# Performance work log

Measured on AMD Instinct MI355X. Metric: run time of the kernel, lower is better.

The kernel has to match this reference:

```python
import jax, jax.numpy as jnp
import numpy as np
from jax import lax

K = 3          # kernel_size
G = 2          # num_groups
DN = ('NHWC', 'HWIO', 'NHWC')


def _conv_same(x, w, b, groups=1):
    y = lax.conv_general_dilated(x, w, (1, 1), 'SAME',
                                 dimension_numbers=DN,
                                 feature_group_count=groups)
    return y + b


def _kernel_grid():
    off = (K - 1) / 2.0
    lin = jnp.linspace(-off, off, K, dtype=jnp.float32)
    dx, dy = jnp.meshgrid(lin, lin)              # 'xy' indexing, like tf default
    return jnp.stack([dx, dy], axis=-1).reshape(K * K, 2)  # [K2, 2] (dx, dy)


def _bilinear_sample(inp, loc):
    # inp: [B,H,W,C], loc: [B,H,W,K2,2] with (x,y) already clipped to valid range
    B, H, W, C = inp.shape
    x, y = loc[..., 0], loc[..., 1]
    x0 = jnp.floor(x); y0 = jnp.floor(y)
    x1 = jnp.clip(x0 + 1.0, 0.0, W - 1.0); x0 = jnp.clip(x0, 0.0, W - 1.0)
    y1 = jnp.clip(y0 + 1.0, 0.0, H - 1.0); y0 = jnp.clip(y0, 0.0, H - 1.0)
    # corner weights (computed from clipped coords, matching the TF code)
    wa = (x1 - x) * (y1 - y)
    wb = (x1 - x) * (y - y0)
    wc = (x - x0) * (y1 - y)
    wd = (x - x0) * (y - y0)
    x0i = x0.astype(jnp.int32); x1i = x1.astype(jnp.int32)
    y0i = y0.astype(jnp.int32); y1i = y1.astype(jnp.int32)
    flat = inp.reshape(B, H * W, C)

    def gather(yi, xi):
        idx = (yi * W + xi).reshape(B, -1, 1)               # [B, H*W*K2, 1]
        v = jnp.take_along_axis(flat, idx, axis=1)          # [B, H*W*K2, C]
        return v.reshape(B, H, W, K * K, C)

    out = (wa[..., None] * gather(y0i, x0i) + wb[..., None] * gather(y1i, x0i)
           + wc[..., None] * gather(y0i, x1i) + wd[..., None] * gather(y1i, x1i))
    return out  # [B,H,W,K2,C]


def _forward(x, off_w, off_b, dw_w, dw_b, pw_w, pw_b):
    B, H, W, C = x.shape
    Cg = C // G
    kg = _kernel_grid()                                     # [K2,2]
    gx, gy = jnp.meshgrid(jnp.arange(W, dtype=jnp.float32),
                          jnp.arange(H, dtype=jnp.float32))
    grid = jnp.stack([gx, gy], axis=-1)                     # [H,W,2] (x,y)
    outs = []
    for g in range(G):
        xi = x[..., g * Cg:(g + 1) * Cg]                    # [B,H,W,Cg]
        offsets = _conv_same(xi, off_w[g], off_b[g])        # [B,H,W,2*K2]
        offsets = offsets.reshape(B, H, W, K * K, 2)
        loc = grid[None, :, :, None, :] + kg[None, None, None] + offsets
        loc = jnp.stack([jnp.clip(loc[..., 0], 0.0, W - 1.0),
                         jnp.clip(loc[..., 1], 0.0, H - 1.0)], axis=-1)
        sampled = _bilinear_sample(xi, loc)                 # [B,H,W,K2,Cg]
        Kin = K * K * Cg
        s = sampled.reshape(B, H, W, Kin)
        s = _conv_same(s, dw_w[g], dw_b[g], groups=Kin)     # depthwise 3x3
        s = _conv_same(s, pw_w[g], pw_b[g])                 # 1x1 pointwise
        outs.append(s)
    return jnp.concatenate(outs, axis=-1)


def setup_inputs() -> dict:
    key = jax.random.key(0)
    ks = jax.random.split(key, 6)
    B, H, W, C = 4, 128, 128, 128
    Cg = C // G
    F = 128
    Fg = F // G
    Kin = K * K * Cg
    x = jax.random.normal(ks[0], (B, H, W, C), jnp.float32)
    # offset conv (zero-init in source; small random weights so offsets ~1px)
    off_w = jax.random.normal(ks[1], (G, K, K, Cg, 2 * K * K), jnp.float32) * 0.05
    off_b = jnp.zeros((G, 2 * K * K), jnp.float32)
    dw_w = jax.random.normal(ks[2], (G, K, K, 1, Kin), jnp.float32) * 0.1
    dw_b = jnp.zeros((G, Kin), jnp.float32)
    pw_w = jax.random.normal(ks[3], (G, 1, 1, Kin, Fg), jnp.float32) / np.sqrt(Kin)
    pw_b = jnp.zeros((G, Fg), jnp.float32)
    return {"x": x, "off_w": off_w, "off_b": off_b,
            "dw_w": dw_w, "dw_b": dw_b, "pw_w": pw_w, "pw_b": pw_b}


def reference(x, off_w, off_b, dw_w, dw_b, pw_w, pw_b):
    return _forward(x, off_w, off_b, dw_w, dw_b, pw_w, pw_b)
```

## Files before the change

kernel.cpp:

```cpp
#include <hip/hip_runtime.h>
#include <hip/hip_bf16.h>

#define HW 128
#define GNUM 2
#define BATCH 4
#define OBT_STRIDE (GNUM * 18 * 2 * 512)
#define PWT_FLOATS 36864
#define OBT_FLOATS 36864
#define DWP_WORDS 5184

typedef short s16x8 __attribute__((ext_vector_type(8)));
typedef _Float16 f16x8 __attribute__((ext_vector_type(8)));
typedef _Float16 f16x2 __attribute__((ext_vector_type(2)));
typedef __fp16 h16x2 __attribute__((ext_vector_type(2)));
typedef float f32x4 __attribute__((ext_vector_type(4)));

__device__ inline unsigned short f2bf(float f) {
    union { float f; unsigned u; } v;
    v.f = f;
    unsigned r = (v.u + 0x7fffu + ((v.u >> 16) & 1u)) >> 16;
    return (unsigned short)r;
}
__device__ inline unsigned pk2bf(float lo, float hi) {
    __hip_bfloat162 r = __float22bfloat162_rn(float2{lo, hi});
    return *(unsigned*)&r;
}
__device__ inline float blo(unsigned u) {
    union { unsigned u; float f; } v; v.u = u << 16; return v.f;
}
__device__ inline float bhi(unsigned u) {
    union { unsigned u; float f; } v; v.u = u & 0xffff0000u; return v.f;
}
__device__ inline unsigned short f2h(float f) {
    _Float16 h = (_Float16)f;
    return *(unsigned short*)&h;
}
__device__ inline unsigned pk2h(float lo, float hi) {
    union { h16x2 h; unsigned u; } v;
    v.h = __builtin_amdgcn_cvt_pkrtz(lo, hi);
    return v.u;
}
__device__ inline f16x2 u2h(unsigned u) {
    union { unsigned u; f16x2 h; } v; v.u = u; return v.h;
}
__device__ inline unsigned h2u(f16x2 h) {
    union { unsigned u; f16x2 h; } v; v.h = h; return v.u;
}
__device__ inline int swz(int row, int off) {
    return (off & 7) | ((((off >> 3) ^ (row + (row >> 3))) & 7) << 3);
}

__global__ __launch_bounds__(256) void prep_kernel(
    const float* __restrict__ pw_w, const float* __restrict__ dw_b,
    const float* __restrict__ off_w, const float* __restrict__ dw_w,
    unsigned short* __restrict__ pwt, unsigned short* __restrict__ obt,
    unsigned* __restrict__ dwp, float* __restrict__ bias2) {
    const int g = blockIdx.y;
    const int t = threadIdx.x;
    if (blockIdx.x < 9) {
        const int j = blockIdx.x;
        const int wv = t >> 6, lane = t & 63;
        const int f = wv * 16 + (lane & 15);
        const int kbase = (lane >> 4) << 3;
#pragma unroll
        for (int ks = 0; ks < 2; ++ks)
#pragma unroll
            for (int i = 0; i < 8; ++i) {
                int kin = j * 64 + ks * 32 + kbase + i;
                pwt[((((g * 9 + j) * 4 + wv) * 2 + ks) << 9) + lane * 8 + i] =
                    f2h(pw_w[(g * 576 + kin) * 64 + f]);
            }
        for (int e = t; e < 288; e += 256) {
            int tap2 = e >> 5, cp = e & 31;
            const float* dwr = &dw_w[(g * 9 + tap2) * 576 + (j << 6) + cp * 2];
            dwp[(((g * 9 + tap2) * 9 + j) << 5) + cp] = pk2h(dwr[0], dwr[1]);
        }
    } else if (blockIdx.x < 27) {
        const int s = blockIdx.x - 9;
        const int tap = s >> 1;
        for (int e = t; e < 1024; e += 256) {
            int nt = e >> 9, le = e & 511;
            int lane = le >> 3, i = le & 7;
            int k = ((lane >> 4) << 3) + i;
            int c = ((s & 1) << 5) + k;
            int n = (nt << 4) + (lane & 15);
            float v = (n < 18) ? off_w[((g * 9 + tap) * 64 + c) * 18 + n] : 0.f;
            unsigned short hi = f2bf(v);
            unsigned short lo = f2bf(v - blo(hi));
            int idx = (((g * 18 + s) * 2 + nt) << 9) + le;
            obt[idx] = hi;
            obt[OBT_STRIDE + idx] = lo;
        }
    } else {
        if (t < 64) {
            float s = 0.f;
            for (int kin = 0; kin < 576; ++kin)
                s += pw_w[(g * 576 + kin) * 64 + t] * dw_b[g * 576 + kin];
            bias2[g * 64 + t] = s;
        }
    }
}

__global__ __launch_bounds__(256, 4) void deform_fused(
    const float* __restrict__ x, const unsigned short* __restrict__ obt,
    const float* __restrict__ off_b, const unsigned* __restrict__ dwp,
    const unsigned short* __restrict__ pwt, const float* __restrict__ bias2,
    const float* __restrict__ pw_b, float* __restrict__ out) {
    __shared__ char smem[32832];
    unsigned short* xh = (unsigned short*)smem;
    unsigned short* samp = (unsigned short*)smem;
    unsigned short* dwa = (unsigned short*)(smem + 12800);
    float* offs = (float*)(smem + 20992);
    float4* wlw = (float4*)(smem + 28192);
    unsigned* wli = (unsigned*)(smem + 29792);

    const int b = blockIdx.x >> 1, g = blockIdx.x & 1;
    const int tileIdx = blockIdx.y;
    const int h0 = (tileIdx >> 4) << 3, w0 = (tileIdx & 15) << 3;
    const int t = threadIdx.x;
    const int lane = t & 63;
    const int wv = __builtin_amdgcn_readfirstlane(t >> 6);
    const int kq = (lane >> 4) << 3;
    const int col = lane & 15;
    const int rq = (lane >> 4) << 2;

    f32x4 oacc[2][2];
#pragma unroll
    for (int sl = 0; sl < 2; ++sl)
#pragma unroll
        for (int nt = 0; nt < 2; ++nt) oacc[sl][nt] = (f32x4){0.f, 0.f, 0.f, 0.f};
    int mbase[2];
#pragma unroll
    for (int sl = 0; sl < 2; ++sl) {
        int mt = wv + (sl << 2);
        int m = mt * 16 + col;
        if (mt < 7 && m < 100) {
            int opy = m / 10, opx = m - opy * 10;
            mbase[sl] = opy * 12 + opx;
        } else
            mbase[sl] = 0;
    }
    for (int q = 0; q < 2; ++q) {
        if (q) __syncthreads();
        for (int idx = t; idx < 144 * 8; idx += 256) {
            int sp = idx >> 3, cq = idx & 7;
            int sy = sp / 12, sx = sp - sy * 12;
            int gy = h0 - 2 + sy, gx = w0 - 2 + sx;
            uint2 hp = {0, 0}, lp = {0, 0};
            if ((unsigned)gy < HW && (unsigned)gx < HW) {
                const float4 v = *(const float4*)&x[(((b * HW + gy) * HW + gx)
                                                    << 7) +
                                                   (g << 6) + (q << 5) + (cq << 2)];
                hp.x = pk2bf(v.x, v.y);
                hp.y = pk2bf(v.z, v.w);
                lp.x = pk2bf(v.x - blo(hp.x), v.y - bhi(hp.x));
                lp.y = pk2bf(v.z - blo(hp.y), v.w - bhi(hp.y));
            }
            *(uint2*)&xh[sp * 64 + swz(sp, cq << 2)] = hp;
            *(uint2*)&xh[sp * 64 + swz(sp, 32 + (cq << 2))] = lp;
        }
        __syncthreads();
        for (int tap = 0; tap < 9; ++tap) {
            const int s = (tap << 1) + q;
            const int ky = tap / 3, kx = tap - ky * 3;
            const int shift = ky * 12 + kx;
            const int bidx = ((g * 18 + s) << 1) << 9;
            s16x8 bh0 = *(const s16x8*)&obt[bidx + lane * 8];
            s16x8 bh1 = *(const s16x8*)&obt[bidx + 512 + lane * 8];
            s16x8 bl0 = *(const s16x8*)&obt[OBT_STRIDE + bidx + lane * 8];
            s16x8 bl1 = *(const s16x8*)&obt[OBT_STRIDE + bidx + 512 + lane * 8];
#pragma unroll
            for (int sl = 0; sl < 2; ++sl) {
                if (wv + (sl << 2) < 7) {
                    const int m2 = mbase[sl] + shift;
                    s16x8 ah = *(const s16x8*)&xh[m2 * 64 + swz(m2, kq)];
                    s16x8 al = *(const s16x8*)&xh[m2 * 64 + swz(m2, kq + 32)];
                    oacc[sl][0] = __builtin_amdgcn_mfma_f32_16x16x32_bf16(
                        ah, bh0, oacc[sl][0], 0, 0, 0);
                    oacc[sl][1] = __builtin_amdgcn_mfma_f32_16x16x32_bf16(
                        ah, bh1, oacc[sl][1], 0, 0, 0);
                    oacc[sl][0] = __builtin_amdgcn_mfma_f32_16x16x32_bf16(
                        al, bh0, oacc[sl][0], 0, 0, 0);
                    oacc[sl][1] = __builtin_amdgcn_mfma_f32_16x16x32_bf16(
                        al, bh1, oacc[sl][1], 0, 0, 0);
                    oacc[sl][0] = __builtin_amdgcn_mfma_f32_16x16x32_bf16(
                        ah, bl0, oacc[sl][0], 0, 0, 0);
                    oacc[sl][1] = __builtin_amdgcn_mfma_f32_16x16x32_bf16(
                        ah, bl1, oacc[sl][1], 0, 0, 0);
                }
            }
        }
    }
#pragma unroll
    for (int sl = 0; sl < 2; ++sl) {
        int mt = wv + (sl << 2);
        if (mt < 7) {
#pragma unroll
            for (int nt = 0; nt < 2; ++nt) {
                int o = (nt << 4) + col;
                if (o < 18) {
                    float ob = off_b[g * 18 + o];
#pragma unroll
                    for (int i = 0; i < 4; ++i) {
                        int m = mt * 16 + rq + i;
                        if (m < 100) offs[m * 18 + o] = oacc[sl][nt][i] + ob;
                    }
                }
            }
        }
    }
    __syncthreads();

    const int fb = wv << 4;
    const int p = lane;
    const int ayp = p >> 3, axp = p & 7;
    const int grp = t >> 4, sl16 = t & 15;
    const int prow = ayp * 10 + axp;

    const float bs = bias2[g * 64 + fb + col] + pw_b[g * 64 + fb + col];
    f32x4 acc[4];
#pragma unroll
    for (int mt = 0; mt < 4; ++mt) acc[mt] = (f32x4){bs, bs, bs, bs};

    for (int j = 0; j < 9; ++j) {
        const int jy = j / 3, jx = j - jy * 3;
        f16x8 bfr[2];
#pragma unroll
        for (int ks = 0; ks < 2; ++ks)
            bfr[ks] = *(const f16x8*)&pwt[((((g * 9 + j) * 4 + wv) * 2 + ks)
                                           << 9) + lane * 8];
        if (t < 100) {
            const int sp = t;
            const int spy = sp / 10, spx = sp - spy * 10;
            const int gy = h0 - 1 + spy, gx = w0 - 1 + spx;
            float4 w4 = {0.f, 0.f, 0.f, 0.f};
            unsigned wp = (unsigned)(b << 21);
            if ((unsigned)gy < HW && (unsigned)gx < HW) {
                const float ox = offs[sp * 18 + 2 * j];
                const float oy = offs[sp * 18 + 2 * j + 1];
                float xf = fminf(fmaxf((float)(gx + jx - 1) + ox, 0.f), 127.f);
                float yf = fminf(fmaxf((float)(gy + jy - 1) + oy, 0.f), 127.f);
                float x0 = floorf(xf), y0 = floorf(yf);
                float x1 = fminf(x0 + 1.f, 127.f);
                float y1 = fminf(y0 + 1.f, 127.f);
                w4.x = (x1 - xf) * (y1 - yf);
                w4.y = (x1 - xf) * (yf - y0);
                w4.z = (xf - x0) * (y1 - yf);
                w4.w = (xf - x0) * (yf - y0);
                const int x0i = (int)x0, y0i = (int)y0;
                wp = (unsigned)(((b * HW + y0i) * HW + x0i) << 7) |
                     (unsigned)((int)x1 - x0i) |
                     ((unsigned)((int)y1 - y0i) << 1);
            }
            wlw[sp] = w4;
            wli[sp] = wp;
        }
        __syncthreads();
        for (int it = 0; it < 7; ++it) {
            const int sp = (it << 4) + grp;
            if (sp < 100) {
                const float4 w4 = wlw[sp];
                const unsigned wp = wli[sp];
                const float* xa = x + (wp & 0xFFFFFF80u) + (g << 6) +
                                  (sl16 << 2);
                const int xo = (int)((wp & 1u) << 7);
                const int yo = (int)((wp & 2u) << 13);
                const float4 va = *(const float4*)xa;
                const float4 vb = *(const float4*)(xa + yo);
                const float4 vc = *(const float4*)(xa + xo);
                const float4 vd = *(const float4*)(xa + xo + yo);
                float r0 = w4.x * va.x + w4.y * vb.x + w4.z * vc.x + w4.w * vd.x;
                float r1 = w4.x * va.y + w4.y * vb.y + w4.z * vc.y + w4.w * vd.y;
                float r2 = w4.x * va.z + w4.y * vb.z + w4.z * vc.z + w4.w * vd.z;
                float r3 = w4.x * va.w + w4.y * vb.w + w4.z * vc.w + w4.w * vd.w;
                uint2 pk;
                pk.x = pk2h(r0, r1);
                pk.y = pk2h(r2, r3);
                *(uint2*)&samp[sp * 64 + swz(sp, sl16 << 2)] = pk;
            }
        }
        __syncthreads();
#pragma unroll
        for (int cq = 0; cq < 2; ++cq) {
            const int c8 = fb + (cq << 3);
            f16x2 d0 = {0, 0}, d1 = {0, 0}, d2 = {0, 0}, d3 = {0, 0};
#pragma unroll
            for (int t2 = 0; t2 < 9; ++t2) {
                const int ky = t2 / 3, kx = t2 - ky * 3;
                const int row = prow + ky * 10 + kx;
                const uint4 hv =
                    *(const uint4*)&samp[row * 64 + swz(row, c8)];
                const uint4 wq =
                    *(const uint4*)&dwp[(((g * 9 + t2) * 9 + j) << 5) +
                                        (c8 >> 1)];
                d0 = u2h(hv.x) * u2h(wq.x) + d0;
                d1 = u2h(hv.y) * u2h(wq.y) + d1;
                d2 = u2h(hv.z) * u2h(wq.z) + d2;
                d3 = u2h(hv.w) * u2h(wq.w) + d3;
            }
            uint4 pk;
            pk.x = h2u(d0);
            pk.y = h2u(d1);
            pk.z = h2u(d2);
            pk.w = h2u(d3);
            *(uint4*)&dwa[p * 64 + swz(p, c8)] = pk;
        }
        __syncthreads();
#pragma unroll
        for (int ks = 0; ks < 2; ++ks)
#pragma unroll
            for (int mt = 0; mt < 4; ++mt) {
                const int row = mt * 16 + col;
                f16x8 af = *(const f16x8*)&dwa[row * 64 +
                                               swz(row, ks * 32 + kq)];
                acc[mt] = __builtin_amdgcn_mfma_f32_16x16x32_f16(
                    af, bfr[ks], acc[mt], 0, 0, 0);
            }
    }
#pragma unroll
    for (int mt = 0; mt < 4; ++mt)
#pragma unroll
        for (int i = 0; i < 4; ++i) {
            int m = mt * 16 + rq + i;
            out[((b * HW + h0 + (m >> 3)) * HW + (w0 + (m & 7))) * 128 +
                (g << 6) + fb + col] = acc[mt][i];
        }
}

extern "C" void kernel_launch(void* const* d_in, const int* in_sizes, int n_in,
                              void* d_out, int out_size, void* d_ws,
                              size_t ws_size, hipStream_t stream) {
    const float* x = (const float*)d_in[0];
    const float* off_w = (const float*)d_in[1];
    const float* off_b = (const float*)d_in[2];
    const float* dw_w = (const float*)d_in[3];
    const float* dw_b = (const float*)d_in[4];
    const float* pw_w = (const float*)d_in[5];
    const float* pw_b = (const float*)d_in[6];

    float* wsf = (float*)d_ws;
    unsigned short* pwt = (unsigned short*)wsf;
    unsigned short* obt = (unsigned short*)(wsf + PWT_FLOATS);
    unsigned* dwp = (unsigned*)(wsf + PWT_FLOATS + OBT_FLOATS);
    float* bias2 = wsf + PWT_FLOATS + OBT_FLOATS + DWP_WORDS;

    prep_kernel<<<dim3(28, GNUM), dim3(256), 0, stream>>>(pw_w, dw_b, off_w,
                                                          dw_w, pwt, obt, dwp,
                                                          bias2);
    deform_fused<<<dim3(BATCH * GNUM, 256), dim3(256), 0, stream>>>(
        x, obt, off_b, dwp, pwt, bias2, pw_b, (float*)d_out);
}
```

Measured before the change: 211.6 us.

## Precompute all bilinear sample tables upfront and hoist LDS address math

Bilinear weights and packed corner indices for all nine kernel taps are now computed once by all threads into a larger shared table. Previously 100 threads recomputed them inside the tap loop, which needed an extra barrier per tap. Swizzled LDS offsets are hoisted into per-thread register arrays, and the sample blend uses 2-wide float vectors. The trade-offs are more shared memory (offs moved to alias the xh region, so a barrier is added) and higher register pressure from the offset arrays, which may reduce occupancy.

```diff
diff --git a/kernel.cpp b/kernel.cpp
--- a/kernel.cpp
+++ b/kernel.cpp
@@ -14,6 +14,7 @@
 typedef _Float16 f16x2 __attribute__((ext_vector_type(2)));
 typedef __fp16 h16x2 __attribute__((ext_vector_type(2)));
 typedef float f32x4 __attribute__((ext_vector_type(4)));
+typedef float f32x2 __attribute__((ext_vector_type(2)));
 
 __device__ inline unsigned short f2bf(float f) {
     union { float f; unsigned u; } v;
@@ -106,13 +107,13 @@
     const float* __restrict__ off_b, const unsigned* __restrict__ dwp,
     const unsigned short* __restrict__ pwt, const float* __restrict__ bias2,
     const float* __restrict__ pw_b, float* __restrict__ out) {
-    __shared__ char smem[32832];
+    __shared__ char smem[38992];
     unsigned short* xh = (unsigned short*)smem;
+    float* offs = (float*)smem;
     unsigned short* samp = (unsigned short*)smem;
     unsigned short* dwa = (unsigned short*)(smem + 12800);
-    float* offs = (float*)(smem + 20992);
-    float4* wlw = (float4*)(smem + 28192);
-    unsigned* wli = (unsigned*)(smem + 29792);
+    float4* wlwAll = (float4*)(smem + 20992);
+    unsigned* wliAll = (unsigned*)(smem + 35392);
 
     const int b = blockIdx.x >> 1, g = blockIdx.x & 1;
     const int tileIdx = blockIdx.y;
@@ -191,6 +192,7 @@
             }
         }
     }
+    __syncthreads();
 #pragma unroll
     for (int sl = 0; sl < 2; ++sl) {
         int mt = wv + (sl << 2);
@@ -210,6 +212,34 @@
         }
     }
     __syncthreads();
+    for (int e = t; e < 900; e += 256) {
+        const int jj = e / 100, sp = e - jj * 100;
+        const int jy = jj / 3, jx = jj - jy * 3;
+        const int spy = sp / 10, spx = sp - spy * 10;
+        const int gy = h0 - 1 + spy, gx = w0 - 1 + spx;
+        float4 w4 = {0.f, 0.f, 0.f, 0.f};
+        unsigned wp = (unsigned)(b << 21);
+        if ((unsigned)gy < HW && (unsigned)gx < HW) {
+            const float ox = offs[sp * 18 + 2 * jj];
+            const float oy = offs[sp * 18 + 2 * jj + 1];
+            float xf = fminf(fmaxf((float)(gx + jx - 1) + ox, 0.f), 127.f);
+            float yf = fminf(fmaxf((float)(gy + jy - 1) + oy, 0.f), 127.f);
+            float x0 = floorf(xf), y0 = floorf(yf);
+            float x1 = fminf(x0 + 1.f, 127.f);
+            float y1 = fminf(y0 + 1.f, 127.f);
+            w4.x = (x1 - xf) * (y1 - yf);
+            w4.y = (x1 - xf) * (yf - y0);
+            w4.z = (xf - x0) * (y1 - yf);
+            w4.w = (xf - x0) * (yf - y0);
+            const int x0i = (int)x0, y0i = (int)y0;
+            wp = (unsigned)(((b * HW + y0i) * HW + x0i) << 7) |
+                 (unsigned)((int)x1 - x0i) |
+                 ((unsigned)((int)y1 - y0i) << 1);
+        }
+        wlwAll[jj * 100 + sp] = w4;
+        wliAll[jj * 100 + sp] = wp;
+    }
+    __syncthreads();
 
     const int fb = wv << 4;
     const int p = lane;
@@ -217,50 +247,49 @@
     const int grp = t >> 4, sl16 = t & 15;
     const int prow = ayp * 10 + axp;
 
+    int aoff[9][2];
+#pragma unroll
+    for (int t2 = 0; t2 < 9; ++t2) {
+        const int ky = t2 / 3, kx = t2 - ky * 3;
+        const int row = prow + ky * 10 + kx;
+#pragma unroll
+        for (int cq = 0; cq < 2; ++cq)
+            aoff[t2][cq] = row * 64 + swz(row, fb + (cq << 3));
+    }
+    int doff[2];
+#pragma unroll
+    for (int cq = 0; cq < 2; ++cq) doff[cq] = p * 64 + swz(p, fb + (cq << 3));
+    int boff[2][4];
+#pragma unroll
+    for (int ks = 0; ks < 2; ++ks)
+#pragma unroll
+        for (int mt = 0; mt < 4; ++mt) {
+            const int row = mt * 16 + col;
+            boff[ks][mt] = row * 64 + swz(row, ks * 32 + kq);
+        }
+    int soff[7];
+#pragma unroll
+    for (int it = 0; it < 7; ++it) {
+        const int sp_ = (it << 4) + grp;
+        soff[it] = sp_ * 64 + swz(sp_, sl16 << 2);
+    }
+
     const float bs = bias2[g * 64 + fb + col] + pw_b[g * 64 + fb + col];
     f32x4 acc[4];
 #pragma unroll
     for (int mt = 0; mt < 4; ++mt) acc[mt] = (f32x4){bs, bs, bs, bs};
 
     for (int j = 0; j < 9; ++j) {
-        const int jy = j / 3, jx = j - jy * 3;
         f16x8 bfr[2];
 #pragma unroll
         for (int ks = 0; ks < 2; ++ks)
             bfr[ks] = *(const f16x8*)&pwt[((((g * 9 + j) * 4 + wv) * 2 + ks)
                                            << 9) + lane * 8];
-        if (t < 100) {
-            const int sp = t;
-            const int spy = sp / 10, spx = sp - spy * 10;
-            const int gy = h0 - 1 + spy, gx = w0 - 1 + spx;
-            float4 w4 = {0.f, 0.f, 0.f, 0.f};
-            unsigned wp = (unsigned)(b << 21);
-            if ((unsigned)gy < HW && (unsigned)gx < HW) {
-                const float ox = offs[sp * 18 + 2 * j];
-                const float oy = offs[sp * 18 + 2 * j + 1];
-                float xf = fminf(fmaxf((float)(gx + jx - 1) + ox, 0.f), 127.f);
-                float yf = fminf(fmaxf((float)(gy + jy - 1) + oy, 0.f), 127.f);
-                float x0 = floorf(xf), y0 = floorf(yf);
-                float x1 = fminf(x0 + 1.f, 127.f);
-                float y1 = fminf(y0 + 1.f, 127.f);
-                w4.x = (x1 - xf) * (y1 - yf);
-                w4.y = (x1 - xf) * (yf - y0);
-                w4.z = (xf - x0) * (y1 - yf);
-                w4.w = (xf - x0) * (yf - y0);
-                const int x0i = (int)x0, y0i = (int)y0;
-                wp = (unsigned)(((b * HW + y0i) * HW + x0i) << 7) |
-                     (unsigned)((int)x1 - x0i) |
-                     ((unsigned)((int)y1 - y0i) << 1);
-            }
-            wlw[sp] = w4;
-            wli[sp] = wp;
-        }
-        __syncthreads();
         for (int it = 0; it < 7; ++it) {
             const int sp = (it << 4) + grp;
             if (sp < 100) {
-                const float4 w4 = wlw[sp];
-                const unsigned wp = wli[sp];
+                const float4 w4 = wlwAll[j * 100 + sp];
+                const unsigned wp = wliAll[j * 100 + sp];
                 const float* xa = x + (wp & 0xFFFFFF80u) + (g << 6) +
                                   (sl16 << 2);
                 const int xo = (int)((wp & 1u) << 7);
@@ -269,14 +298,16 @@
                 const float4 vb = *(const float4*)(xa + yo);
                 const float4 vc = *(const float4*)(xa + xo);
                 const float4 vd = *(const float4*)(xa + xo + yo);
-                float r0 = w4.x * va.x + w4.y * vb.x + w4.z * vc.x + w4.w * vd.x;
-                float r1 = w4.x * va.y + w4.y * vb.y + w4.z * vc.y + w4.w * vd.y;
-                float r2 = w4.x * va.z + w4.y * vb.z + w4.z * vc.z + w4.w * vd.z;
-                float r3 = w4.x * va.w + w4.y * vb.w + w4.z * vc.w + w4.w * vd.w;
+                f32x2 a01 = {va.x, va.y}, b01 = {vb.x, vb.y};
+                f32x2 c01 = {vc.x, vc.y}, d01 = {vd.x, vd.y};
+                f32x2 a23 = {va.z, va.w}, b23 = {vb.z, vb.w};
+                f32x2 c23 = {vc.z, vc.w}, d23 = {vd.z, vd.w};
+                f32x2 r01 = w4.x * a01 + w4.y * b01 + w4.z * c01 + w4.w * d01;
+                f32x2 r23 = w4.x * a23 + w4.y * b23 + w4.z * c23 + w4.w * d23;
                 uint2 pk;
-                pk.x = pk2h(r0, r1);
-                pk.y = pk2h(r2, r3);
-                *(uint2*)&samp[sp * 64 + swz(sp, sl16 << 2)] = pk;
+                pk.x = pk2h(r01.x, r01.y);
+                pk.y = pk2h(r23.x, r23.y);
+                *(uint2*)&samp[soff[it]] = pk;
             }
         }
         __syncthreads();
@@ -286,10 +317,7 @@
             f16x2 d0 = {0, 0}, d1 = {0, 0}, d2 = {0, 0}, d3 = {0, 0};
 #pragma unroll
             for (int t2 = 0; t2 < 9; ++t2) {
-                const int ky = t2 / 3, kx = t2 - ky * 3;
-                const int row = prow + ky * 10 + kx;
-                const uint4 hv =
-                    *(const uint4*)&samp[row * 64 + swz(row, c8)];
+                const uint4 hv = *(const uint4*)&samp[aoff[t2][cq]];
                 const uint4 wq =
                     *(const uint4*)&dwp[(((g * 9 + t2) * 9 + j) << 5) +
                                         (c8 >> 1)];
@@ -303,16 +331,14 @@
             pk.y = h2u(d1);
             pk.z = h2u(d2);
             pk.w = h2u(d3);
-            *(uint4*)&dwa[p * 64 + swz(p, c8)] = pk;
+            *(uint4*)&dwa[doff[cq]] = pk;
         }
         __syncthreads();
 #pragma unroll
         for (int ks = 0; ks < 2; ++ks)
 #pragma unroll
             for (int mt = 0; mt < 4; ++mt) {
-                const int row = mt * 16 + col;
-                f16x8 af = *(const f16x8*)&dwa[row * 64 +
-                                               swz(row, ks * 32 + kq)];
+                f16x8 af = *(const f16x8*)&dwa[boff[ks][mt]];
                 acc[mt] = __builtin_amdgcn_mfma_f32_16x16x32_f16(
                     af, bfr[ks], acc[mt], 0, 0, 0);
             }
```

New measurement: 209.1 us. No clear change (-1.2%).
